# Kernel tuning notes

Measured on AMD Instinct MI355X. Metric: run time of the kernel, lower is better.

## Reference

```python
import jax, jax.numpy as jnp
import numpy as np

B, T, H, W, C = 2, 4, 128, 128, 192
HEADS = 6
WS = 8          # attention window (per-frame, wsD=1)
OW = 12         # overlapping KV window: 8 + int(8*0.5)
PAD = (OW - WS) // 2
TBL = (WS + OW - 1) ** 2   # 361 relative-position-bias entries
MLP_HID = C * 2


def setup_inputs() -> dict:
    key = jax.random.key(0)
    ks = jax.random.split(key, 8)
    s = 0.02
    return dict(
        x=jax.random.normal(ks[0], (B, T, H, W, C), jnp.float32),
        x_size=jnp.array([H, W], jnp.int32),  # unused by forward (shadowed), kept for signature fidelity
        rpi_oca=jax.random.randint(ks[1], (WS * WS, OW * OW), 0, TBL),
        norm1_g=jnp.ones((C,), jnp.float32), norm1_b=jnp.zeros((C,), jnp.float32),
        qkv_w=jax.random.normal(ks[2], (C, 3 * C), jnp.float32) * s,
        qkv_b=jnp.zeros((3 * C,), jnp.float32),
        rpb_table=jax.random.normal(ks[3], (TBL, HEADS), jnp.float32) * s,
        norm2_g=jnp.ones((C,), jnp.float32), norm2_b=jnp.zeros((C,), jnp.float32),
        fc1_w=jax.random.normal(ks[4], (C, MLP_HID), jnp.float32) * s,
        fc1_b=jnp.zeros((MLP_HID,), jnp.float32),
        fc2_w=jax.random.normal(ks[5], (MLP_HID, C), jnp.float32) * s,
        fc2_b=jnp.zeros((C,), jnp.float32),
    )


def _ln(x, g, b):
    m = x.mean(-1, keepdims=True)
    v = ((x - m) ** 2).mean(-1, keepdims=True)
    return (x - m) * jax.lax.rsqrt(v + 1e-5) * g + b


def reference(x, x_size, rpi_oca, norm1_g, norm1_b, qkv_w, qkv_b, rpb_table,
              norm2_g, norm2_b, fc1_w, fc1_b, fc2_w, fc2_b):
    b, t, h, w, c = x.shape
    d = c // HEADS
    scale = d ** -0.5
    nH, nW = h // WS, w // WS
    b_ = b * t * nH * nW  # total windows
    shortcut = x
    xn = _ln(x, norm1_g, norm1_b)
    qkv = (xn @ qkv_w + qkv_b).reshape(b, t, h, w, 3, c)
    q, k, v = qkv[..., 0, :], qkv[..., 1, :], qkv[..., 2, :]
    # --- query: non-overlapping (1,8,8) windows -> (b_, heads, 64, d)
    qw = (q.reshape(b, t, nH, WS, nW, WS, c)
           .transpose(0, 1, 2, 4, 3, 5, 6)
           .reshape(b_, WS * WS, HEADS, d)
           .transpose(0, 2, 1, 3))
    # --- key/value: overlapping (1,12,12) windows with stride 8, zero-padded by 2
    hid = (jnp.arange(nH) * WS)[:, None] + jnp.arange(OW)  # (nH, OW)
    wid = (jnp.arange(nW) * WS)[:, None] + jnp.arange(OW)  # (nW, OW)

    def owin(z):
        zp = jnp.pad(z, ((0, 0), (0, 0), (PAD, PAD), (PAD, PAD), (0, 0)))
        zw = zp[:, :, hid][:, :, :, :, wid]  # (b, t, nH, OW, nW, OW, c)
        return (zw.transpose(0, 1, 2, 4, 3, 5, 6)
                  .reshape(b_, OW * OW, HEADS, d)
                  .transpose(0, 2, 1, 3))

    kw, vw = owin(k), owin(v)
    attn = jnp.einsum('bhqd,bhkd->bhqk', qw * scale, kw)  # (b_, heads, 64, 144)
    bias = rpb_table[rpi_oca.reshape(-1)].reshape(WS * WS, OW * OW, HEADS).transpose(2, 0, 1)
    attn = attn + bias[None]  # NOTE: original forward applies NO softmax (self.softmax unused)
    out = (jnp.einsum('bhqk,bhkd->bhqd', attn, vw)
             .transpose(0, 2, 1, 3)
             .reshape(b_, WS * WS, c))
    # window_reverse
    xa = (out.reshape(b, t, nH, nW, WS, WS, c)
             .transpose(0, 1, 2, 4, 3, 5, 6)
             .reshape(b, t, h, w, c))
    x = xa + shortcut  # self.proj is never applied in the original forward
    hmlp = jax.nn.gelu(_ln(x, norm2_g, norm2_b) @ fc1_w + fc1_b, approximate=False)
    return x + (hmlp @ fc2_w + fc2_b)
```

## Files before the change

### kernel.cpp

```cpp
#include <hip/hip_runtime.h>
#include <cstdint>
#include <cstddef>

typedef short bf16x8 __attribute__((ext_vector_type(8)));
typedef unsigned short u16x4 __attribute__((ext_vector_type(4)));
typedef float f32x4  __attribute__((ext_vector_type(4)));
typedef unsigned short u16;

#define DEVI __device__ __forceinline__

constexpr int C     = 192;
constexpr int HEADS = 6;
constexpr int NQKV  = 576;
constexpr int HID   = 384;
constexpr int NTOK  = 131072;

DEVI u16 f2bf(float f){
  union { float f; unsigned u; } v; v.f = f;
  return (u16)((v.u + 0x7fffu + ((v.u >> 16) & 1u)) >> 16);
}
DEVI float bf2f(u16 h){
  union { unsigned u; float f; } v; v.u = ((unsigned)h) << 16;
  return v.f;
}

DEVI float gelu(float xx){
  float y  = xx * 0.70710678118654752f;
  float ay = fabsf(y);
  float t  = __builtin_amdgcn_rcpf(1.0f + 0.3275911f * ay);
  float p  = t*(0.254829592f + t*(-0.284496736f + t*(1.421413741f + t*(-1.453152027f + t*1.061405429f))));
  float e  = __expf(-(y*y));
  float er = copysignf(1.0f - p*e, y);
  return 0.5f * xx * (1.0f + er);
}

__global__ void prep_kernel(const float* __restrict__ qkv_w,
                            const float* __restrict__ fc1_w,
                            const float* __restrict__ fc2_w,
                            const int*   __restrict__ rpi,
                            const float* __restrict__ rpb,
                            u16* __restrict__ qkvP,
                            u16* __restrict__ fc1P,
                            u16* __restrict__ fc2P,
                            float* __restrict__ bias_pk){
  int idx = blockIdx.x * blockDim.x + threadIdx.x;
  int stride = gridDim.x * blockDim.x;
  for(int i = idx; i < 36*6*64*8; i += stride){
    int e = i & 7, lane = (i >> 3) & 63, t = i >> 9;
    int ks = t % 6, p = t / 6;
    int n = p*16 + (lane & 15), k = ks*32 + (lane >> 4)*8 + e;
    qkvP[i] = f2bf(qkv_w[k*NQKV + n]);
  }
  for(int i = idx; i < 24*6*64*8; i += stride){
    int e = i & 7, lane = (i >> 3) & 63, t = i >> 9;
    int ks = t % 6, p = t / 6;
    int n = p*16 + (lane & 15), k = ks*32 + (lane >> 4)*8 + e;
    fc1P[i] = f2bf(fc1_w[k*HID + n]);
  }
  for(int i = idx; i < 12*12*64*8; i += stride){
    int e = i & 7, lane = (i >> 3) & 63, t = i >> 9;
    int ks = t % 12, p = t / 12;
    int n = p*16 + (lane & 15), k = ks*32 + (lane >> 4)*8 + e;
    fc2P[i] = f2bf(fc2_w[k*C + n]);
  }
  const int n4 = HEADS*5*2*4*64*4;
  for(int i = idx; i < n4; i += stride){
    int t = i;
    int r    = t & 3;  t >>= 2;
    int lane = t & 63; t >>= 6;
    int mi   = t & 3;  t >>= 2;
    int nf   = t & 1;  t >>= 1;
    int chunk = t % 5; int head = t / 5;
    int q  = mi*16 + (lane & 15);
    int kk = chunk*32 + nf*16 + ((lane >> 4) << 2) + r;
    float v = 0.f;
    if(kk < 144) v = rpb[rpi[q*144 + kk]*HEADS + head];
    bias_pk[i] = v;
  }
}

__global__ __launch_bounds__(384, 4)
void qkv_kernel(const float* __restrict__ x,
                const float* __restrict__ g1,
                const float* __restrict__ b1,
                const u16* __restrict__ wP,
                const float* __restrict__ qb,
                u16* __restrict__ qkv){
  __shared__ u16 xn[64][200];
  __shared__ u16 rp[64][152];
  const int tid = threadIdx.x;
  const int bid = blockIdx.x;
  const int nh = (bid >> 3) & 1;
  const int tb = (bid & 7) + ((bid >> 4) << 3);
  const size_t tok0 = (size_t)tb * 64;
  if(tid < 256){
    const int trow = tid >> 2;
    const int j = tid & 3;
    const float* xr = x + (tok0 + trow)*C;
    float4 xv[12];
    #pragma unroll
    for(int u = 0; u < 12; ++u)
      xv[u] = *reinterpret_cast<const float4*>(xr + u*16 + j*4);
    float s1 = 0.f, s2 = 0.f;
    #pragma unroll
    for(int u = 0; u < 12; ++u){
      const float* f = reinterpret_cast<const float*>(&xv[u]);
      #pragma unroll
      for(int e = 0; e < 4; ++e){ s1 += f[e]; s2 += f[e]*f[e]; }
    }
    s1 += __shfl_xor(s1, 1, 64); s2 += __shfl_xor(s2, 1, 64);
    s1 += __shfl_xor(s1, 2, 64); s2 += __shfl_xor(s2, 2, 64);
    const float mean = s1 * (1.f/192.f);
    const float rstd = rsqrtf(s2*(1.f/192.f) - mean*mean + 1e-5f);
    #pragma unroll
    for(int u = 0; u < 12; ++u){
      const float4 gv = *reinterpret_cast<const float4*>(g1 + u*16 + j*4);
      const float4 bv = *reinterpret_cast<const float4*>(b1 + u*16 + j*4);
      const float* f = reinterpret_cast<const float*>(&xv[u]);
      const float* gp = reinterpret_cast<const float*>(&gv);
      const float* bp = reinterpret_cast<const float*>(&bv);
      u16x4 pk;
      #pragma unroll
      for(int e = 0; e < 4; ++e) pk[e] = f2bf((f[e] - mean)*rstd*gp[e] + bp[e]);
      *reinterpret_cast<u16x4*>(&xn[trow][u*16 + j*4]) = pk;
    }
  }
  __syncthreads();
  const int lane = tid & 63;
  const int wn = tid >> 6;
  const int g = lane >> 4, col = lane & 15;
  const f32x4 fzero = {0.f, 0.f, 0.f, 0.f};
  f32x4 acc[4][3];
  #pragma unroll
  for(int mi = 0; mi < 4; ++mi)
    #pragma unroll
    for(int nf = 0; nf < 3; ++nf) acc[mi][nf] = fzero;
  const int p0 = nh*18 + wn*3;
  #pragma unroll
  for(int ks = 0; ks < 6; ++ks){
    bf16x8 wf[3];
    #pragma unroll
    for(int nf = 0; nf < 3; ++nf)
      wf[nf] = *reinterpret_cast<const bf16x8*>(wP + ((size_t)(((p0 + nf)*6 + ks)*64) + lane)*8);
    bf16x8 a[4];
    #pragma unroll
    for(int mi = 0; mi < 4; ++mi)
      a[mi] = *reinterpret_cast<const bf16x8*>(&xn[mi*16 + col][ks*32 + g*8]);
    #pragma unroll
    for(int nf = 0; nf < 3; ++nf)
      #pragma unroll
      for(int mi = 0; mi < 4; ++mi)
        acc[mi][nf] = __builtin_amdgcn_mfma_f32_16x16x32_bf16(a[mi], wf[nf], acc[mi][nf], 0, 0, 0);
  }
  #pragma unroll
  for(int ph = 0; ph < 2; ++ph){
    if(wn >= ph*3 && wn < ph*3 + 3){
      const int wl = wn - ph*3;
      #pragma unroll
      for(int mi = 0; mi < 4; ++mi){
        #pragma unroll
        for(int nf = 0; nf < 3; ++nf){
          const int nloc = wl*48 + nf*16 + col;
          const float bb = qb[nh*288 + ph*144 + nloc];
          #pragma unroll
          for(int r = 0; r < 4; ++r)
            rp[mi*16 + g*4 + r][nloc] = f2bf(acc[mi][nf][r] + bb);
        }
      }
    }
    __syncthreads();
    #pragma unroll
    for(int it = 0; it < 3; ++it){
      const int c = tid + it*384;
      const int tok = c / 18, cc = c - tok*18;
      const int n0 = nh*288 + ph*144 + cc*8;
      const int pl = n0 >> 5, d0 = n0 & 31;
      bf16x8 vv = *reinterpret_cast<const bf16x8*>(&rp[tok][cc*8]);
      *reinterpret_cast<bf16x8*>(qkv + ((size_t)pl*NTOK + tok0 + tok)*32 + d0) = vv;
    }
    __syncthreads();
  }
}

template<bool X1B>
__global__ __launch_bounds__(256, 5)
void attn_kernel(const u16* __restrict__ qkv,
                 const float* __restrict__ bias_pk,
                 const float* __restrict__ x,
                 float* __restrict__ out,
                 u16* __restrict__ x1b){
  __shared__ alignas(16) char smem[28672];
  u16 (*Kl)[40]  = reinterpret_cast<u16(*)[40]>(smem);
  u16 (*Vt)[168] = reinterpret_cast<u16(*)[168]>(smem + 12800);
  char* Plb      = smem + 23552;
  float (*Of)[36] = reinterpret_cast<float(*)[36]>(smem);
  const int tid  = threadIdx.x;
  const int lane = tid & 63;
  const int w    = tid >> 6;
  const int g = lane >> 4, col = lane & 15;
  const int win = blockIdx.x, head = blockIdx.y;
  const int bt = win >> 8, wh = (win >> 4) & 15, ww = win & 15;
  const int h0 = wh*8, w0 = ww*8;
  const size_t tokbase = (size_t)bt * 16384;
  const u16* Qp = qkv + (size_t)head      *NTOK*32;
  const u16* Kp = qkv + (size_t)(6 + head)*NTOK*32;
  const u16* Vp = qkv + (size_t)(12 + head)*NTOK*32;
  const bf16x8 z8 = {0,0,0,0,0,0,0,0};

  #pragma unroll
  for(int ii = 0; ii < 3; ++ii){
    const int i = w + ii*4;
    if(i < 10){
      const int kr = i*16 + col;
      const int r12 = (kr*2731) >> 15;
      const int c12 = kr - r12*12;
      const int hh = h0 - 2 + r12;
      const int wp = w0 - 2 + c12;
      const bool valid = (kr < 144) && (hh >= 0) && (hh < 128) && (wp >= 0) && (wp < 128);
      const size_t t = valid ? (tokbase + (size_t)hh*128 + wp) : tokbase;
      bf16x8 kv_ = *reinterpret_cast<const bf16x8*>(Kp + t*32 + g*8);
      bf16x8 vv_ = *reinterpret_cast<const bf16x8*>(Vp + t*32 + g*8);
      kv_ = valid ? kv_ : z8;
      vv_ = valid ? vv_ : z8;
      *reinterpret_cast<bf16x8*>(&Kl[kr][g*8]) = kv_;
      #pragma unroll
      for(int e = 0; e < 8; ++e) Vt[g*8 + e][kr] = (u16)vv_[e];
    }
  }
  bf16x8 qf;
  {
    const int row = w*16 + col;
    const size_t t = tokbase + (size_t)(h0 + (row >> 3))*128 + (w0 + (row & 7));
    qf = *reinterpret_cast<const bf16x8*>(Qp + t*32 + g*8);
  }
  __syncthreads();

  const f32x4 fzero = {0.f, 0.f, 0.f, 0.f};
  f32x4 oacc[2];
  oacc[0] = fzero; oacc[1] = fzero;
  const float scale = 0.17677669529663689f;

  #pragma unroll
  for(int ch = 0; ch < 5; ++ch){
    float4 bv[2];
    #pragma unroll
    for(int nf = 0; nf < 2; ++nf)
      bv[nf] = *reinterpret_cast<const float4*>(
          bias_pk + (size_t)((((head*5 + ch)*2 + nf)*4 + w)*64 + lane)*4);
    bf16x8 kfr[2];
    #pragma unroll
    for(int nf = 0; nf < 2; ++nf)
      kfr[nf] = *reinterpret_cast<const bf16x8*>(&Kl[ch*32 + nf*16 + col][g*8]);
    f32x4 st[2];
    #pragma unroll
    for(int nf = 0; nf < 2; ++nf)
      st[nf] = __builtin_amdgcn_mfma_f32_16x16x32_bf16(kfr[nf], qf, fzero, 0, 0, 0);
    #pragma unroll
    for(int nf = 0; nf < 2; ++nf){
      const float* bp = reinterpret_cast<const float*>(&bv[nf]);
      const float p0 = fmaf(st[nf][0], scale, bp[0]);
      const float p1 = fmaf(st[nf][1], scale, bp[1]);
      const float p2 = fmaf(st[nf][2], scale, bp[2]);
      const float p3 = fmaf(st[nf][3], scale, bp[3]);
      uint2 pw;
      pw.x = (unsigned)f2bf(p0) | ((unsigned)f2bf(p1) << 16);
      pw.y = (unsigned)f2bf(p2) | ((unsigned)f2bf(p3) << 16);
      *reinterpret_cast<uint2*>(Plb + (w*16 + col)*80 + nf*32 + g*8) = pw;
    }
    bf16x8 pa = *reinterpret_cast<const bf16x8*>(Plb + (w*16 + col)*80 + g*16);
    bf16x8 vfr[2];
    #pragma unroll
    for(int nf = 0; nf < 2; ++nf)
      vfr[nf] = *reinterpret_cast<const bf16x8*>(&Vt[nf*16 + col][ch*32 + g*8]);
    #pragma unroll
    for(int nf = 0; nf < 2; ++nf)
      oacc[nf] = __builtin_amdgcn_mfma_f32_16x16x32_bf16(pa, vfr[nf], oacc[nf], 0, 0, 0);
  }
  __syncthreads();
  #pragma unroll
  for(int nf = 0; nf < 2; ++nf)
    #pragma unroll
    for(int r = 0; r < 4; ++r)
      Of[w*16 + g*4 + r][nf*16 + col] = oacc[nf][r];
  __syncthreads();
  {
    const int tok = tid >> 2, q = tid & 3;
    const int hh = h0 + (tok >> 3), wp = w0 + (tok & 7);
    const size_t trow = tokbase + (size_t)hh*128 + wp;
    const size_t o = trow*(size_t)C + head*32 + q*8;
    float4 a0 = *reinterpret_cast<const float4*>(&Of[tok][q*8]);
    float4 a1 = *reinterpret_cast<const float4*>(&Of[tok][q*8 + 4]);
    const float4 x0 = *reinterpret_cast<const float4*>(x + o);
    const float4 x1 = *reinterpret_cast<const float4*>(x + o + 4);
    a0.x += x0.x; a0.y += x0.y; a0.z += x0.z; a0.w += x0.w;
    a1.x += x1.x; a1.y += x1.y; a1.z += x1.z; a1.w += x1.w;
    if(X1B){
      bf16x8 pk;
      pk[0] = (short)f2bf(a0.x); pk[1] = (short)f2bf(a0.y);
      pk[2] = (short)f2bf(a0.z); pk[3] = (short)f2bf(a0.w);
      pk[4] = (short)f2bf(a1.x); pk[5] = (short)f2bf(a1.y);
      pk[6] = (short)f2bf(a1.z); pk[7] = (short)f2bf(a1.w);
      *reinterpret_cast<bf16x8*>(x1b + o) = pk;
    }else{
      *reinterpret_cast<float4*>(out + o)     = a0;
      *reinterpret_cast<float4*>(out + o + 4) = a1;
    }
  }
}

template<bool X1B>
__global__ __launch_bounds__(512, 4)
void mlp_kernel(float* __restrict__ io,
                const u16* __restrict__ x1b,
                const float* __restrict__ g2,
                const float* __restrict__ b2,
                const u16* __restrict__ w1P,
                const float* __restrict__ fb1,
                const u16* __restrict__ w2P,
                const float* __restrict__ fb2){
  __shared__ u16 xn[64][200];
  __shared__ u16 hl[64][200];
  const int tid = threadIdx.x;
  const size_t tok0 = (size_t)blockIdx.x * 64;
  {
    const int trow = tid >> 3;
    const int j = tid & 7;
    float v[24];
    if(X1B){
      const u16* xr = x1b + (tok0 + trow)*C + j*24;
      bf16x8 b0 = *reinterpret_cast<const bf16x8*>(xr);
      bf16x8 b1 = *reinterpret_cast<const bf16x8*>(xr + 8);
      bf16x8 b2_ = *reinterpret_cast<const bf16x8*>(xr + 16);
      #pragma unroll
      for(int e = 0; e < 8; ++e){ v[e] = bf2f((u16)b0[e]); v[8+e] = bf2f((u16)b1[e]); v[16+e] = bf2f((u16)b2_[e]); }
    }else{
      const float* xr = io + (tok0 + trow)*C;
      #pragma unroll
      for(int u = 0; u < 6; ++u){
        const float4 t = *reinterpret_cast<const float4*>(xr + u*32 + j*4);
        v[u*4+0] = t.x; v[u*4+1] = t.y; v[u*4+2] = t.z; v[u*4+3] = t.w;
      }
    }
    float s1 = 0.f, s2 = 0.f;
    #pragma unroll
    for(int e = 0; e < 24; ++e){ s1 += v[e]; s2 += v[e]*v[e]; }
    s1 += __shfl_xor(s1, 1, 64); s2 += __shfl_xor(s2, 1, 64);
    s1 += __shfl_xor(s1, 2, 64); s2 += __shfl_xor(s2, 2, 64);
    s1 += __shfl_xor(s1, 4, 64); s2 += __shfl_xor(s2, 4, 64);
    const float mean = s1 * (1.f/192.f);
    const float rstd = rsqrtf(s2*(1.f/192.f) - mean*mean + 1e-5f);
    if(X1B){
      #pragma unroll
      for(int u = 0; u < 6; ++u){
        const float4 gv = *reinterpret_cast<const float4*>(g2 + j*24 + u*4);
        const float4 bv = *reinterpret_cast<const float4*>(b2 + j*24 + u*4);
        const float* gp = reinterpret_cast<const float*>(&gv);
        const float* bp = reinterpret_cast<const float*>(&bv);
        u16x4 pk;
        #pragma unroll
        for(int e = 0; e < 4; ++e) pk[e] = f2bf((v[u*4+e] - mean)*rstd*gp[e] + bp[e]);
        *reinterpret_cast<u16x4*>(&xn[trow][j*24 + u*4]) = pk;
      }
    }else{
      #pragma unroll
      for(int u = 0; u < 6; ++u){
        const float4 gv = *reinterpret_cast<const float4*>(g2 + u*32 + j*4);
        const float4 bv = *reinterpret_cast<const float4*>(b2 + u*32 + j*4);
        const float* gp = reinterpret_cast<const float*>(&gv);
        const float* bp = reinterpret_cast<const float*>(&bv);
        u16x4 pk;
        #pragma unroll
        for(int e = 0; e < 4; ++e) pk[e] = f2bf((v[u*4+e] - mean)*rstd*gp[e] + bp[e]);
        *reinterpret_cast<u16x4*>(&xn[trow][u*32 + j*4]) = pk;
      }
    }
  }
  __syncthreads();
  const int lane = tid & 63, wave = tid >> 6;
  const int wm = wave >> 2;
  const int wn = wave & 3;
  const int g = lane >> 4, col = lane & 15;
  const f32x4 fzero = {0.f, 0.f, 0.f, 0.f};
  f32x4 acc2[2][3];
  #pragma unroll
  for(int mi = 0; mi < 2; ++mi)
    #pragma unroll
    for(int nf = 0; nf < 3; ++nf) acc2[mi][nf] = fzero;
  #pragma unroll
  for(int hb = 0; hb < 2; ++hb){
    f32x4 acc1[2][3];
    #pragma unroll
    for(int mi = 0; mi < 2; ++mi)
      #pragma unroll
      for(int nf = 0; nf < 3; ++nf) acc1[mi][nf] = fzero;
    #pragma unroll
    for(int ks = 0; ks < 6; ++ks){
      bf16x8 wf[3];
      #pragma unroll
      for(int nf = 0; nf < 3; ++nf)
        wf[nf] = *reinterpret_cast<const bf16x8*>(w1P + ((size_t)(((hb*12 + wn*3 + nf)*6 + ks)*64) + lane)*8);
      bf16x8 a[2];
      #pragma unroll
      for(int mi = 0; mi < 2; ++mi)
        a[mi] = *reinterpret_cast<const bf16x8*>(&xn[wm*32 + mi*16 + col][ks*32 + g*8]);
      #pragma unroll
      for(int nf = 0; nf < 3; ++nf)
        #pragma unroll
        for(int mi = 0; mi < 2; ++mi)
          acc1[mi][nf] = __builtin_amdgcn_mfma_f32_16x16x32_bf16(a[mi], wf[nf], acc1[mi][nf], 0, 0, 0);
    }
    #pragma unroll
    for(int mi = 0; mi < 2; ++mi){
      #pragma unroll
      for(int nf = 0; nf < 3; ++nf){
        const int nl = wn*48 + nf*16 + col;
        const float bb = fb1[hb*192 + nl];
        #pragma unroll
        for(int r = 0; r < 4; ++r){
          const int row = wm*32 + mi*16 + g*4 + r;
          hl[row][nl] = f2bf(gelu(acc1[mi][nf][r] + bb));
        }
      }
    }
    __syncthreads();
    #pragma unroll
    for(int ks = 0; ks < 6; ++ks){
      bf16x8 wf[3];
      #pragma unroll
      for(int nf = 0; nf < 3; ++nf)
        wf[nf] = *reinterpret_cast<const bf16x8*>(w2P + ((size_t)(((wn*3 + nf)*12 + hb*6 + ks)*64) + lane)*8);
      bf16x8 a[2];
      #pragma unroll
      for(int mi = 0; mi < 2; ++mi)
        a[mi] = *reinterpret_cast<const bf16x8*>(&hl[wm*32 + mi*16 + col][ks*32 + g*8]);
      #pragma unroll
      for(int nf = 0; nf < 3; ++nf)
        #pragma unroll
        for(int mi = 0; mi < 2; ++mi)
          acc2[mi][nf] = __builtin_amdgcn_mfma_f32_16x16x32_bf16(a[mi], wf[nf], acc2[mi][nf], 0, 0, 0);
    }
    __syncthreads();
  }
  if(X1B){
    #pragma unroll
    for(int mi = 0; mi < 2; ++mi){
      #pragma unroll
      for(int nf = 0; nf < 3; ++nf){
        const int n = wn*48 + nf*16 + col;
        const float bb = fb2[n];
        #pragma unroll
        for(int r = 0; r < 4; ++r){
          const int row = wm*32 + mi*16 + g*4 + r;
          xn[row][n] = f2bf(acc2[mi][nf][r] + bb);
        }
      }
    }
    __syncthreads();
    const int trow = tid >> 3, j = tid & 7;
    const u16* xq = x1b + (tok0 + trow)*C + j*24;
    float* op = io + (tok0 + trow)*C + j*24;
    bf16x8 r0 = *reinterpret_cast<const bf16x8*>(xq);
    bf16x8 r1 = *reinterpret_cast<const bf16x8*>(xq + 8);
    bf16x8 r2 = *reinterpret_cast<const bf16x8*>(xq + 16);
    bf16x8 m0 = *reinterpret_cast<const bf16x8*>(&xn[trow][j*24]);
    bf16x8 m1 = *reinterpret_cast<const bf16x8*>(&xn[trow][j*24 + 8]);
    bf16x8 m2 = *reinterpret_cast<const bf16x8*>(&xn[trow][j*24 + 16]);
    float ov[24];
    #pragma unroll
    for(int e = 0; e < 8; ++e){
      ov[e]    = bf2f((u16)r0[e]) + bf2f((u16)m0[e]);
      ov[8+e]  = bf2f((u16)r1[e]) + bf2f((u16)m1[e]);
      ov[16+e] = bf2f((u16)r2[e]) + bf2f((u16)m2[e]);
    }
    #pragma unroll
    for(int u = 0; u < 6; ++u){
      float4 t; t.x = ov[u*4]; t.y = ov[u*4+1]; t.z = ov[u*4+2]; t.w = ov[u*4+3];
      *reinterpret_cast<float4*>(op + u*4) = t;
    }
  }else{
    #pragma unroll
    for(int mi = 0; mi < 2; ++mi){
      #pragma unroll
      for(int nf = 0; nf < 3; ++nf){
        const int n = wn*48 + nf*16 + col;
        const float bb = fb2[n];
        #pragma unroll
        for(int r = 0; r < 4; ++r){
          const int row = wm*32 + mi*16 + g*4 + r;
          const size_t idx = (tok0 + row)*C + n;
          io[idx] = acc2[mi][nf][r] + bb + io[idx];
        }
      }
    }
  }
}

extern "C" void kernel_launch(void* const* d_in, const int* in_sizes, int n_in,
                              void* d_out, int out_size, void* d_ws, size_t ws_size,
                              hipStream_t stream){
  const float* x    = (const float*)d_in[0];
  const int*   rpi  = (const int*)  d_in[2];
  const float* n1g  = (const float*)d_in[3];
  const float* n1b  = (const float*)d_in[4];
  const float* qkvw = (const float*)d_in[5];
  const float* qkvb = (const float*)d_in[6];
  const float* rpb  = (const float*)d_in[7];
  const float* n2g  = (const float*)d_in[8];
  const float* n2b  = (const float*)d_in[9];
  const float* fc1w = (const float*)d_in[10];
  const float* fc1b = (const float*)d_in[11];
  const float* fc2w = (const float*)d_in[12];
  const float* fc2b = (const float*)d_in[13];
  float* out = (float*)d_out;
  char* ws = (char*)d_ws;
  u16*   qkvP    = (u16*)  (ws + 0);
  u16*   fc1P    = (u16*)  (ws + 221184);
  u16*   fc2P    = (u16*)  (ws + 368640);
  float* bias_pk = (float*)(ws + 516096);
  u16*   qkvbuf  = (u16*)  (ws + 1499136);
  u16*   x1b     = (u16*)  (ws + 152494080);
  if(ws_size < 152494080ull) return;
  const bool big = ws_size >= 202825728ull;
  prep_kernel<<<dim3(512), dim3(256), 0, stream>>>(qkvw, fc1w, fc2w, rpi, rpb, qkvP, fc1P, fc2P, bias_pk);
  qkv_kernel<<<dim3(4096), dim3(384), 0, stream>>>(x, n1g, n1b, qkvP, qkvb, qkvbuf);
  if(big){
    attn_kernel<true><<<dim3(2048, 6), dim3(256), 0, stream>>>(qkvbuf, bias_pk, x, out, x1b);
    mlp_kernel<true><<<dim3(2048), dim3(512), 0, stream>>>(out, x1b, n2g, n2b, fc1P, fc1b, fc2P, fc2b);
  }else{
    attn_kernel<false><<<dim3(2048, 6), dim3(256), 0, stream>>>(qkvbuf, bias_pk, x, out, nullptr);
    mlp_kernel<false><<<dim3(2048), dim3(512), 0, stream>>>(out, nullptr, n2g, n2b, fc1P, fc1b, fc2P, fc2b);
  }
}
```

Measured before the change: 284.0 us.

## Shrink MLP tile to 32 tokens and compute full hidden layer in one pass

```diff
diff --git a/kernel.cpp b/kernel.cpp
--- a/kernel.cpp
+++ b/kernel.cpp
@@ -309,7 +309,7 @@
 }
 
 template<bool X1B>
-__global__ __launch_bounds__(512, 4)
+__global__ __launch_bounds__(256, 4)
 void mlp_kernel(float* __restrict__ io,
                 const u16* __restrict__ x1b,
                 const float* __restrict__ g2,
@@ -318,10 +318,10 @@
                 const float* __restrict__ fb1,
                 const u16* __restrict__ w2P,
                 const float* __restrict__ fb2){
-  __shared__ u16 xn[64][200];
-  __shared__ u16 hl[64][200];
+  __shared__ u16 xn[32][200];
+  __shared__ u16 hl[32][392];
   const int tid = threadIdx.x;
-  const size_t tok0 = (size_t)blockIdx.x * 64;
+  const size_t tok0 = (size_t)blockIdx.x * 32;
   {
     const int trow = tid >> 3;
     const int j = tid & 7;
@@ -334,10 +334,10 @@
       #pragma unroll
       for(int e = 0; e < 8; ++e){ v[e] = bf2f((u16)b0[e]); v[8+e] = bf2f((u16)b1[e]); v[16+e] = bf2f((u16)b2_[e]); }
     }else{
-      const float* xr = io + (tok0 + trow)*C;
+      const float* xr = io + (tok0 + trow)*C + j*24;
       #pragma unroll
       for(int u = 0; u < 6; ++u){
-        const float4 t = *reinterpret_cast<const float4*>(xr + u*32 + j*4);
+        const float4 t = *reinterpret_cast<const float4*>(xr + u*4);
         v[u*4+0] = t.x; v[u*4+1] = t.y; v[u*4+2] = t.z; v[u*4+3] = t.w;
       }
     }
@@ -349,108 +349,88 @@
     s1 += __shfl_xor(s1, 4, 64); s2 += __shfl_xor(s2, 4, 64);
     const float mean = s1 * (1.f/192.f);
     const float rstd = rsqrtf(s2*(1.f/192.f) - mean*mean + 1e-5f);
-    if(X1B){
-      #pragma unroll
-      for(int u = 0; u < 6; ++u){
-        const float4 gv = *reinterpret_cast<const float4*>(g2 + j*24 + u*4);
-        const float4 bv = *reinterpret_cast<const float4*>(b2 + j*24 + u*4);
-        const float* gp = reinterpret_cast<const float*>(&gv);
-        const float* bp = reinterpret_cast<const float*>(&bv);
-        u16x4 pk;
-        #pragma unroll
-        for(int e = 0; e < 4; ++e) pk[e] = f2bf((v[u*4+e] - mean)*rstd*gp[e] + bp[e]);
-        *reinterpret_cast<u16x4*>(&xn[trow][j*24 + u*4]) = pk;
-      }
-    }else{
-      #pragma unroll
-      for(int u = 0; u < 6; ++u){
-        const float4 gv = *reinterpret_cast<const float4*>(g2 + u*32 + j*4);
-        const float4 bv = *reinterpret_cast<const float4*>(b2 + u*32 + j*4);
-        const float* gp = reinterpret_cast<const float*>(&gv);
-        const float* bp = reinterpret_cast<const float*>(&bv);
-        u16x4 pk;
-        #pragma unroll
-        for(int e = 0; e < 4; ++e) pk[e] = f2bf((v[u*4+e] - mean)*rstd*gp[e] + bp[e]);
-        *reinterpret_cast<u16x4*>(&xn[trow][u*32 + j*4]) = pk;
-      }
+    #pragma unroll
+    for(int u = 0; u < 6; ++u){
+      const float4 gv = *reinterpret_cast<const float4*>(g2 + j*24 + u*4);
+      const float4 bv = *reinterpret_cast<const float4*>(b2 + j*24 + u*4);
+      const float* gp = reinterpret_cast<const float*>(&gv);
+      const float* bp = reinterpret_cast<const float*>(&bv);
+      u16x4 pk;
+      #pragma unroll
+      for(int e = 0; e < 4; ++e) pk[e] = f2bf((v[u*4+e] - mean)*rstd*gp[e] + bp[e]);
+      *reinterpret_cast<u16x4*>(&xn[trow][j*24 + u*4]) = pk;
     }
   }
   __syncthreads();
-  const int lane = tid & 63, wave = tid >> 6;
-  const int wm = wave >> 2;
-  const int wn = wave & 3;
+  const int lane = tid & 63, w = tid >> 6;
   const int g = lane >> 4, col = lane & 15;
   const f32x4 fzero = {0.f, 0.f, 0.f, 0.f};
+  f32x4 acc1[2][6];
+  #pragma unroll
+  for(int mi = 0; mi < 2; ++mi)
+    #pragma unroll
+    for(int nf = 0; nf < 6; ++nf) acc1[mi][nf] = fzero;
+  #pragma unroll
+  for(int ks = 0; ks < 6; ++ks){
+    bf16x8 wf[6];
+    #pragma unroll
+    for(int nf = 0; nf < 6; ++nf)
+      wf[nf] = *reinterpret_cast<const bf16x8*>(w1P + ((size_t)(((w*6 + nf)*6 + ks)*64) + lane)*8);
+    bf16x8 a[2];
+    #pragma unroll
+    for(int mi = 0; mi < 2; ++mi)
+      a[mi] = *reinterpret_cast<const bf16x8*>(&xn[mi*16 + col][ks*32 + g*8]);
+    #pragma unroll
+    for(int nf = 0; nf < 6; ++nf)
+      #pragma unroll
+      for(int mi = 0; mi < 2; ++mi)
+        acc1[mi][nf] = __builtin_amdgcn_mfma_f32_16x16x32_bf16(a[mi], wf[nf], acc1[mi][nf], 0, 0, 0);
+  }
+  #pragma unroll
+  for(int mi = 0; mi < 2; ++mi){
+    #pragma unroll
+    for(int nf = 0; nf < 6; ++nf){
+      const int nl = w*96 + nf*16 + col;
+      const float bb = fb1[nl];
+      #pragma unroll
+      for(int r = 0; r < 4; ++r){
+        const int row = mi*16 + g*4 + r;
+        hl[row][nl] = f2bf(gelu(acc1[mi][nf][r] + bb));
+      }
+    }
+  }
+  __syncthreads();
   f32x4 acc2[2][3];
   #pragma unroll
   for(int mi = 0; mi < 2; ++mi)
     #pragma unroll
     for(int nf = 0; nf < 3; ++nf) acc2[mi][nf] = fzero;
   #pragma unroll
-  for(int hb = 0; hb < 2; ++hb){
-    f32x4 acc1[2][3];
+  for(int ks = 0; ks < 12; ++ks){
+    bf16x8 wf[3];
+    #pragma unroll
+    for(int nf = 0; nf < 3; ++nf)
+      wf[nf] = *reinterpret_cast<const bf16x8*>(w2P + ((size_t)(((w*3 + nf)*12 + ks)*64) + lane)*8);
+    bf16x8 a[2];
     #pragma unroll
     for(int mi = 0; mi < 2; ++mi)
-      #pragma unroll
-      for(int nf = 0; nf < 3; ++nf) acc1[mi][nf] = fzero;
-    #pragma unroll
-    for(int ks = 0; ks < 6; ++ks){
-      bf16x8 wf[3];
-      #pragma unroll
-      for(int nf = 0; nf < 3; ++nf)
-        wf[nf] = *reinterpret_cast<const bf16x8*>(w1P + ((size_t)(((hb*12 + wn*3 + nf)*6 + ks)*64) + lane)*8);
-      bf16x8 a[2];
+      a[mi] = *reinterpret_cast<const bf16x8*>(&hl[mi*16 + col][ks*32 + g*8]);
+    #pragma unroll
+    for(int nf = 0; nf < 3; ++nf)
       #pragma unroll
       for(int mi = 0; mi < 2; ++mi)
-        a[mi] = *reinterpret_cast<const bf16x8*>(&xn[wm*32 + mi*16 + col][ks*32 + g*8]);
-      #pragma unroll
-      for(int nf = 0; nf < 3; ++nf)
-        #pragma unroll
-        for(int mi = 0; mi < 2; ++mi)
-          acc1[mi][nf] = __builtin_amdgcn_mfma_f32_16x16x32_bf16(a[mi], wf[nf], acc1[mi][nf], 0, 0, 0);
-    }
+        acc2[mi][nf] = __builtin_amdgcn_mfma_f32_16x16x32_bf16(a[mi], wf[nf], acc2[mi][nf], 0, 0, 0);
+  }
+  if(X1B){
     #pragma unroll
     for(int mi = 0; mi < 2; ++mi){
       #pragma unroll
       for(int nf = 0; nf < 3; ++nf){
-        const int nl = wn*48 + nf*16 + col;
-        const float bb = fb1[hb*192 + nl];
-        #pragma unroll
-        for(int r = 0; r < 4; ++r){
-          const int row = wm*32 + mi*16 + g*4 + r;
-          hl[row][nl] = f2bf(gelu(acc1[mi][nf][r] + bb));
-        }
-      }
-    }
-    __syncthreads();
-    #pragma unroll
-    for(int ks = 0; ks < 6; ++ks){
-      bf16x8 wf[3];
-      #pragma unroll
-      for(int nf = 0; nf < 3; ++nf)
-        wf[nf] = *reinterpret_cast<const bf16x8*>(w2P + ((size_t)(((wn*3 + nf)*12 + hb*6 + ks)*64) + lane)*8);
-      bf16x8 a[2];
-      #pragma unroll
-      for(int mi = 0; mi < 2; ++mi)
-        a[mi] = *reinterpret_cast<const bf16x8*>(&hl[wm*32 + mi*16 + col][ks*32 + g*8]);
-      #pragma unroll
-      for(int nf = 0; nf < 3; ++nf)
-        #pragma unroll
-        for(int mi = 0; mi < 2; ++mi)
-          acc2[mi][nf] = __builtin_amdgcn_mfma_f32_16x16x32_bf16(a[mi], wf[nf], acc2[mi][nf], 0, 0, 0);
-    }
-    __syncthreads();
-  }
-  if(X1B){
-    #pragma unroll
-    for(int mi = 0; mi < 2; ++mi){
-      #pragma unroll
-      for(int nf = 0; nf < 3; ++nf){
-        const int n = wn*48 + nf*16 + col;
+        const int n = w*48 + nf*16 + col;
         const float bb = fb2[n];
         #pragma unroll
         for(int r = 0; r < 4; ++r){
-          const int row = wm*32 + mi*16 + g*4 + r;
+          const int row = mi*16 + g*4 + r;
           xn[row][n] = f2bf(acc2[mi][nf][r] + bb);
         }
       }
@@ -482,11 +462,11 @@
     for(int mi = 0; mi < 2; ++mi){
       #pragma unroll
       for(int nf = 0; nf < 3; ++nf){
-        const int n = wn*48 + nf*16 + col;
+        const int n = w*48 + nf*16 + col;
         const float bb = fb2[n];
         #pragma unroll
         for(int r = 0; r < 4; ++r){
-          const int row = wm*32 + mi*16 + g*4 + r;
+          const int row = mi*16 + g*4 + r;
           const size_t idx = (tok0 + row)*C + n;
           io[idx] = acc2[mi][nf][r] + bb + io[idx];
         }
@@ -525,9 +505,9 @@
   qkv_kernel<<<dim3(4096), dim3(384), 0, stream>>>(x, n1g, n1b, qkvP, qkvb, qkvbuf);
   if(big){
     attn_kernel<true><<<dim3(2048, 6), dim3(256), 0, stream>>>(qkvbuf, bias_pk, x, out, x1b);
-    mlp_kernel<true><<<dim3(2048), dim3(512), 0, stream>>>(out, x1b, n2g, n2b, fc1P, fc1b, fc2P, fc2b);
+    mlp_kernel<true><<<dim3(4096), dim3(256), 0, stream>>>(out, x1b, n2g, n2b, fc1P, fc1b, fc2P, fc2b);
   }else{
     attn_kernel<false><<<dim3(2048, 6), dim3(256), 0, stream>>>(qkvbuf, bias_pk, x, out, nullptr);
-    mlp_kernel<false><<<dim3(2048), dim3(512), 0, stream>>>(out, nullptr, n2g, n2b, fc1P, fc1b, fc2P, fc2b);
-  }
-}
+    mlp_kernel<false><<<dim3(4096), dim3(256), 0, stream>>>(out, nullptr, n2g, n2b, fc1P, fc1b, fc2P, fc2b);
+  }
+}
```

After: 274.4 us. -3.4%, faster.
